# Kernel optimization log

Hardware: AMD Instinct MI355X
Metric: run time of the kernel (lower is better)

## Reference

```python
import jax, jax.numpy as jnp
import numpy as np

B, NCOL, NCOND = 1024, 64, 64
NRODT, D, NEST, NFOREST, NHID, NCLASS = 1024, 4, 128, 100, 128, 10
EPS = 1e-5


def setup_inputs() -> dict:
    key = jax.random.key(0)
    ks = jax.random.split(key, 16)
    rng = np.random.default_rng(0)
    s = 0.1
    inp = {
        'x': jax.random.normal(ks[0], (B, NCOL), jnp.float32),
        # phi_1 numerical grouped conv: groups=NCOL, in_per_g=1, out_per_g=NCOND
        'w1': jax.random.normal(ks[1], (NCOL, 1, NCOND), jnp.float32) * s,
        'b1': jax.random.normal(ks[2], (NCOL * NCOND,), jnp.float32) * s,
        # rODTConstruction fixed permutation of the 4096 conditions
        'perm': jnp.asarray(rng.permutation(NCOND * NCOL), jnp.int32),
        'gn1_g': jnp.ones((NCOND * NCOL,), jnp.float32),
        'gn1_b': jnp.zeros((NCOND * NCOL,), jnp.float32),
        # phi_2 grouped convs: groups=NRODT, block D->D then D->1
        'w2a': jax.random.normal(ks[3], (NRODT, D, D), jnp.float32) * s,
        'b2a': jax.random.normal(ks[4], (NRODT * D,), jnp.float32) * s,
        'gn2_g': jnp.ones((NCOND * NCOL,), jnp.float32),
        'gn2_b': jnp.zeros((NCOND * NCOL,), jnp.float32),
        'w2b': jax.random.normal(ks[5], (NRODT, D, 1), jnp.float32) * s,
        'b2b': jax.random.normal(ks[6], (NRODT,), jnp.float32) * s,
        'E': jax.random.normal(ks[7], (NRODT, NHID), jnp.float32) * s,
        # eval-mode sample_without_replacement buffer: per-forest subset of rODTs
        'swr': jnp.asarray(np.argsort(rng.random((NFOREST, NRODT)), axis=-1)[:, :NEST], jnp.int32),
        'ln1_g': jnp.ones((NHID,), jnp.float32),
        'ln1_b': jnp.zeros((NHID,), jnp.float32),
        'lin1_w': jax.random.normal(ks[8], (NHID, NHID), jnp.float32) * s,
        'lin1_b': jax.random.normal(ks[9], (NHID,), jnp.float32) * s,
        'ln2_g': jnp.ones((NHID,), jnp.float32),
        'ln2_b': jnp.zeros((NHID,), jnp.float32),
        'lin2_w': jax.random.normal(ks[10], (NHID, NCLASS), jnp.float32) * s,
        'lin2_b': jax.random.normal(ks[11], (NCLASS,), jnp.float32) * s,
    }
    return inp


def _group_norm(v, g, gamma, beta):
    # v: (B, C), normalize within each of g channel groups (L=1 in the torch module)
    b, c = v.shape
    vg = v.reshape(b, g, c // g)
    mu = vg.mean(-1, keepdims=True)
    var = vg.var(-1, keepdims=True)
    vn = ((vg - mu) / jnp.sqrt(var + EPS)).reshape(b, c)
    return vn * gamma + beta


def _layer_norm(v, gamma, beta):
    mu = v.mean(-1, keepdims=True)
    var = v.var(-1, keepdims=True)
    return (v - mu) / jnp.sqrt(var + EPS) * gamma + beta


def reference(x, w1, b1, perm, gn1_g, gn1_b, w2a, b2a, gn2_g, gn2_b, w2b, b2b,
              E, swr, ln1_g, ln1_b, lin1_w, lin1_b, ln2_g, ln2_b, lin2_w, lin2_b):
    b = x.shape[0]
    # ConditionGeneration (numerical only): block-diag GEMV with in_per_group=1
    M = jax.nn.sigmoid(x[:, :, None] * w1[None, :, 0, :] + b1.reshape(NCOL, NCOND))  # (B, NCOL, NCOND)
    M = M.transpose(0, 2, 1)  # (B, NCOND, NCOL)
    # rODTConstruction: flatten + fixed permutation
    O = M.reshape(b, NCOND * NCOL)[:, perm]  # (B, 4096)
    # phi_2: GroupNorm -> grouped conv (D->D) -> ReLU -> GroupNorm -> grouped conv (D->1)
    h = _group_norm(O, NRODT, gn1_g, gn1_b).reshape(b, NRODT, D)
    h = jnp.einsum('bgi,gio->bgo', h, w2a) + b2a.reshape(NRODT, D)
    h = jax.nn.relu(h).reshape(b, NRODT * D)
    h = _group_norm(h, NRODT, gn2_g, gn2_b).reshape(b, NRODT, D)
    w = jnp.einsum('bgi,gio->bgo', h, w2b)[..., 0] + b2b  # (B, NRODT), n_head=1
    # forest construction: gather rODT subsets, softmax over estimators, weighted embed sum
    ws = jax.nn.softmax(w[:, swr], axis=-1)  # (B, NFOREST, NEST)
    Es = E[swr]  # (NFOREST, NEST, NHID)
    F = jnp.einsum('bfe,feh->bfh', ws, Es)  # (B, NFOREST, NHID)
    # phi_3 bagging MLP (eval mode: dropout = identity)
    z = _layer_norm(F, ln1_g, ln1_b)
    z = jax.nn.relu(z @ lin1_w + lin1_b)
    z = _layer_norm(z, ln2_g, ln2_b)
    y_hats = z @ lin2_w + lin2_b  # (B, NFOREST, NCLASS)
    return y_hats.mean(1)  # (B, NCLASS)
```

## Files before the change

kernel.cpp:

```cpp
#include <hip/hip_runtime.h>


#define B_      1024
#define NCOL_   64
#define NCOND_  64
#define NRODT_  1024
#define NEST_   128
#define NFOREST_ 100
#define NHID_   128
#define NCLASS_ 10
#define EPS_    1e-5f

typedef __bf16 bf16_t;
typedef bf16_t bf16x8 __attribute__((ext_vector_type(8)));
typedef float  f32x4  __attribute__((ext_vector_type(4)));

#define MFMA16(a,b,c) __builtin_amdgcn_mfma_f32_16x16x32_bf16(a,b,c,0,0,0)

#define EG_FRAGS   (NFOREST_*4*8*64)
#define W1_FRAGS   (4*8*64)
#define L2_FRAGS   (4*64)

__global__ __launch_bounds__(256) void k_prep(
    const float* __restrict__ E,     const int*   __restrict__ swr,
    const float* __restrict__ lin1w, const float* __restrict__ lin2w,
    const float* __restrict__ x,
    bf16_t* __restrict__ Eh,  bf16_t* __restrict__ El,
    bf16_t* __restrict__ Wh,  bf16_t* __restrict__ Wl,
    bf16_t* __restrict__ L2h, bf16_t* __restrict__ L2l,
    float*  __restrict__ x_t, float* __restrict__ accz)
{
    int blk = blockIdx.x, tid = threadIdx.x;
    if (blk < 800) {
        int t = blk * 256 + tid;
        int lane = t & 63, nn = (t >> 6) & 7, kk = (t >> 9) & 3, f = t >> 11;
        int q = lane >> 4, n = nn * 16 + (lane & 15);
        bf16x8 hi, lo;
#pragma unroll
        for (int j = 0; j < 8; ++j) {
            int e = kk * 32 + q * 8 + j;
            int r = swr[f * NEST_ + e];
            float v = E[r * NHID_ + n];
            bf16_t h = (bf16_t)v;
            hi[j] = h; lo[j] = (bf16_t)(v - (float)h);
        }
        *(bf16x8*)(Eh + (size_t)t * 8) = hi;
        *(bf16x8*)(El + (size_t)t * 8) = lo;
    } else if (blk < 808) {
        int t = (blk - 800) * 256 + tid;
        int lane = t & 63, nn = (t >> 6) & 7, kk = t >> 9;
        int q = lane >> 4, n = nn * 16 + (lane & 15);
        bf16x8 hi, lo;
#pragma unroll
        for (int j = 0; j < 8; ++j) {
            int k = kk * 32 + q * 8 + j;
            float v = lin1w[k * NHID_ + n];
            bf16_t h = (bf16_t)v;
            hi[j] = h; lo[j] = (bf16_t)(v - (float)h);
        }
        *(bf16x8*)(Wh + t * 8) = hi;
        *(bf16x8*)(Wl + t * 8) = lo;
    } else if (blk == 808) {
        int t = tid;
        int lane = t & 63, kk = t >> 6;
        int q = lane >> 4, n = lane & 15;
        bf16x8 hi, lo;
#pragma unroll
        for (int j = 0; j < 8; ++j) {
            int k = kk * 32 + q * 8 + j;
            float v = (n < NCLASS_) ? lin2w[k * NCLASS_ + n] : 0.f;
            bf16_t h = (bf16_t)v;
            hi[j] = h; lo[j] = (bf16_t)(v - (float)h);
        }
        *(bf16x8*)(L2h + t * 8) = hi;
        *(bf16x8*)(L2l + t * 8) = lo;
    } else if (blk < 1065) {
        int t = (blk - 809) * 256 + tid;
        x_t[t] = x[(t & 1023) * NCOL_ + (t >> 10)];
    } else {
        int t = (blk - 1065) * 256 + tid;
        if (t < B_ * NCLASS_) accz[t] = 0.f;
    }
}

__global__ __launch_bounds__(256) void k_rodt(
    const float* __restrict__ x_t,  const float* __restrict__ w1,
    const float* __restrict__ b1,   const int*  __restrict__ perm,
    const float* __restrict__ gn1g, const float* __restrict__ gn1b,
    const float* __restrict__ w2a,  const float* __restrict__ b2a,
    const float* __restrict__ gn2g, const float* __restrict__ gn2b,
    const float* __restrict__ w2b,  const float* __restrict__ b2b,
    float* __restrict__ w_t)
{
    int g  = blockIdx.x;
    int bq = threadIdx.x * 4;

    int4 p4 = ((const int4*)perm)[g];
    int col[4]  = { p4.x & 63, p4.y & 63, p4.z & 63, p4.w & 63 };
    int cond[4] = { p4.x >> 6, p4.y >> 6, p4.z >> 6, p4.w >> 6 };
    float w1v[4], b1v[4];
#pragma unroll
    for (int j = 0; j < 4; ++j) {
        w1v[j] = w1[col[j] * NCOND_ + cond[j]];
        b1v[j] = b1[col[j] * NCOND_ + cond[j]];
    }
    float4 g1  = ((const float4*)gn1g)[g];
    float4 o1  = ((const float4*)gn1b)[g];
    float4 ba  = ((const float4*)b2a)[g];
    float4 g2  = ((const float4*)gn2g)[g];
    float4 o2  = ((const float4*)gn2b)[g];
    float4 wb4 = ((const float4*)w2b)[g];
    float  bb  = b2b[g];
    float4 wa[4];
    const float4* w2a4 = (const float4*)w2a;
#pragma unroll
    for (int i = 0; i < 4; ++i) wa[i] = w2a4[g * 4 + i];

    float xv[4][4];
#pragma unroll
    for (int j = 0; j < 4; ++j) {
        float4 t = *(const float4*)&x_t[col[j] * B_ + bq];
        xv[j][0] = t.x; xv[j][1] = t.y; xv[j][2] = t.z; xv[j][3] = t.w;
    }

    float outv[4];
#pragma unroll
    for (int bi = 0; bi < 4; ++bi) {
        float v[4];
#pragma unroll
        for (int j = 0; j < 4; ++j) {
            float t = xv[j][bi] * w1v[j] + b1v[j];
            v[j] = 1.0f / (1.0f + __expf(-t));
        }
        float mu = (v[0] + v[1] + v[2] + v[3]) * 0.25f;
        float var = 0.f;
#pragma unroll
        for (int j = 0; j < 4; ++j) { float d = v[j] - mu; var += d * d; }
        var *= 0.25f;
        float rs = rsqrtf(var + EPS_);
        float h[4];
        h[0] = (v[0] - mu) * rs * g1.x + o1.x;
        h[1] = (v[1] - mu) * rs * g1.y + o1.y;
        h[2] = (v[2] - mu) * rs * g1.z + o1.z;
        h[3] = (v[3] - mu) * rs * g1.w + o1.w;

        float4 a = ba;
#pragma unroll
        for (int i = 0; i < 4; ++i) {
            a.x += h[i] * wa[i].x; a.y += h[i] * wa[i].y;
            a.z += h[i] * wa[i].z; a.w += h[i] * wa[i].w;
        }
        float t2[4];
        t2[0] = fmaxf(a.x, 0.f); t2[1] = fmaxf(a.y, 0.f);
        t2[2] = fmaxf(a.z, 0.f); t2[3] = fmaxf(a.w, 0.f);

        float mu2 = (t2[0] + t2[1] + t2[2] + t2[3]) * 0.25f;
        float var2 = 0.f;
#pragma unroll
        for (int j = 0; j < 4; ++j) { float d = t2[j] - mu2; var2 += d * d; }
        var2 *= 0.25f;
        float rs2 = rsqrtf(var2 + EPS_);

        float wvv = bb;
        wvv += ((t2[0] - mu2) * rs2 * g2.x + o2.x) * wb4.x;
        wvv += ((t2[1] - mu2) * rs2 * g2.y + o2.y) * wb4.y;
        wvv += ((t2[2] - mu2) * rs2 * g2.z + o2.z) * wb4.z;
        wvv += ((t2[3] - mu2) * rs2 * g2.w + o2.w) * wb4.w;
        outv[bi] = wvv;
    }
    *(float4*)&w_t[(size_t)g * B_ + bq] = make_float4(outv[0], outv[1], outv[2], outv[3]);
}

__global__ __launch_bounds__(256, 4) void k_forest(
    const float*  __restrict__ w_t, const int* __restrict__ swr,
    const bf16_t* __restrict__ Eh,  const bf16_t* __restrict__ El,
    const bf16_t* __restrict__ Wh,  const bf16_t* __restrict__ Wl,
    const bf16_t* __restrict__ L2h, const bf16_t* __restrict__ L2l,
    const float* __restrict__ ln1g, const float* __restrict__ ln1b,
    const float* __restrict__ lin1b,
    const float* __restrict__ ln2g, const float* __restrict__ ln2b,
    float* __restrict__ acc)
{
    __shared__ float zsh[4][16 * 132];

    int tid  = threadIdx.x;
    int wid  = tid >> 6;
    int lane = tid & 63;
    int q    = lane >> 4;
    int mc   = lane & 15;

    int n    = blockIdx.x;
    int swiz = (n & 7) * 200 + (n >> 3);
    int f    = swiz >> 4;
    int bt   = swiz & 15;
    int b0   = bt * 64 + wid * 16;

    const int* swrf = swr + f * NEST_;
    float* zw = zsh[wid];

    float ex[4][8];
    float mx = -1e30f;
#pragma unroll
    for (int kk = 0; kk < 4; ++kk) {
        int4 r0 = *(const int4*)(swrf + kk * 32 + q * 8);
        int4 r1 = *(const int4*)(swrf + kk * 32 + q * 8 + 4);
        int rr[8] = { r0.x, r0.y, r0.z, r0.w, r1.x, r1.y, r1.z, r1.w };
#pragma unroll
        for (int j = 0; j < 8; ++j) {
            float v = w_t[rr[j] * B_ + b0 + mc];
            ex[kk][j] = v;
            mx = fmaxf(mx, v);
        }
    }
    mx = fmaxf(mx, __shfl_xor(mx, 16));
    mx = fmaxf(mx, __shfl_xor(mx, 32));
    float s = 0.f;
#pragma unroll
    for (int kk = 0; kk < 4; ++kk)
#pragma unroll
        for (int j = 0; j < 8; ++j) { ex[kk][j] = __expf(ex[kk][j] - mx); s += ex[kk][j]; }
    s += __shfl_xor(s, 16);
    s += __shfl_xor(s, 32);
    float inv = 1.f / s;

    bf16x8 afr[4];
#pragma unroll
    for (int kk = 0; kk < 4; ++kk)
#pragma unroll
        for (int j = 0; j < 8; ++j) afr[kk][j] = (bf16_t)(ex[kk][j] * inv);

    f32x4 accF[8];
#pragma unroll
    for (int nn = 0; nn < 8; ++nn) accF[nn] = (f32x4){0.f, 0.f, 0.f, 0.f};
    const bf16x8* EHf = (const bf16x8*)Eh;
    const bf16x8* ELf = (const bf16x8*)El;
#pragma unroll
    for (int kk = 0; kk < 4; ++kk) {
        size_t bi = (size_t)(f * 4 + kk) * 8;
#pragma unroll
        for (int nn = 0; nn < 8; ++nn) {
            bf16x8 bh = EHf[(bi + nn) * 64 + lane];
            bf16x8 bl = ELf[(bi + nn) * 64 + lane];
            accF[nn] = MFMA16(afr[kk], bh, accF[nn]);
            accF[nn] = MFMA16(afr[kk], bl, accF[nn]);
        }
    }

    float mu[4], rs[4];
#pragma unroll
    for (int reg = 0; reg < 4; ++reg) {
        float ps = 0.f, pq = 0.f;
#pragma unroll
        for (int nn = 0; nn < 8; ++nn) { float v = accF[nn][reg]; ps += v; pq += v * v; }
#pragma unroll
        for (int o = 1; o <= 8; o <<= 1) { ps += __shfl_xor(ps, o); pq += __shfl_xor(pq, o); }
        float m_ = ps * (1.f / NHID_);
        mu[reg] = m_;
        rs[reg] = rsqrtf(pq * (1.f / NHID_) - m_ * m_ + EPS_);
    }
    {
#pragma unroll
        for (int nn = 0; nn < 8; ++nn) {
            int c = nn * 16 + mc;
            float gv = ln1g[c], bv = ln1b[c];
#pragma unroll
            for (int reg = 0; reg < 4; ++reg)
                zw[(q * 4 + reg) * 132 + c] = (accF[nn][reg] - mu[reg]) * rs[reg] * gv + bv;
        }
    }

    bf16x8 a2[4];
#pragma unroll
    for (int kk = 0; kk < 4; ++kk) {
        int dwb = kk * 32 + q * 8;
        f32x4 u0 = *(const f32x4*)&zw[mc * 132 + dwb];
        f32x4 u1 = *(const f32x4*)&zw[mc * 132 + dwb + 4];
#pragma unroll
        for (int j = 0; j < 4; ++j) { a2[kk][j] = (bf16_t)u0[j]; a2[kk][4 + j] = (bf16_t)u1[j]; }
    }
    f32x4 accA[8];
#pragma unroll
    for (int nn = 0; nn < 8; ++nn) accA[nn] = (f32x4){0.f, 0.f, 0.f, 0.f};
    const bf16x8* WHf = (const bf16x8*)Wh;
    const bf16x8* WLf = (const bf16x8*)Wl;
#pragma unroll
    for (int kk = 0; kk < 4; ++kk) {
#pragma unroll
        for (int nn = 0; nn < 8; ++nn) {
            bf16x8 bh = WHf[(kk * 8 + nn) * 64 + lane];
            bf16x8 bl = WLf[(kk * 8 + nn) * 64 + lane];
            accA[nn] = MFMA16(a2[kk], bh, accA[nn]);
            accA[nn] = MFMA16(a2[kk], bl, accA[nn]);
        }
    }

#pragma unroll
    for (int nn = 0; nn < 8; ++nn) {
        float bv = lin1b[nn * 16 + mc];
#pragma unroll
        for (int reg = 0; reg < 4; ++reg)
            accA[nn][reg] = fmaxf(accA[nn][reg] + bv, 0.f);
    }
    float mu2[4], rs2[4];
#pragma unroll
    for (int reg = 0; reg < 4; ++reg) {
        float ps = 0.f, pq = 0.f;
#pragma unroll
        for (int nn = 0; nn < 8; ++nn) { float v = accA[nn][reg]; ps += v; pq += v * v; }
#pragma unroll
        for (int o = 1; o <= 8; o <<= 1) { ps += __shfl_xor(ps, o); pq += __shfl_xor(pq, o); }
        float m_ = ps * (1.f / NHID_);
        mu2[reg] = m_;
        rs2[reg] = rsqrtf(pq * (1.f / NHID_) - m_ * m_ + EPS_);
    }
    {
#pragma unroll
        for (int nn = 0; nn < 8; ++nn) {
            int c = nn * 16 + mc;
            float gv = ln2g[c], bv = ln2b[c];
#pragma unroll
            for (int reg = 0; reg < 4; ++reg)
                zw[(q * 4 + reg) * 132 + c] = (accA[nn][reg] - mu2[reg]) * rs2[reg] * gv + bv;
        }
    }

    f32x4 accO = {0.f, 0.f, 0.f, 0.f};
    const bf16x8* LHf = (const bf16x8*)L2h;
    const bf16x8* LLf = (const bf16x8*)L2l;
#pragma unroll
    for (int kk = 0; kk < 4; ++kk) {
        int dwb = kk * 32 + q * 8;
        f32x4 u0 = *(const f32x4*)&zw[mc * 132 + dwb];
        f32x4 u1 = *(const f32x4*)&zw[mc * 132 + dwb + 4];
        bf16x8 a3;
#pragma unroll
        for (int j = 0; j < 4; ++j) { a3[j] = (bf16_t)u0[j]; a3[4 + j] = (bf16_t)u1[j]; }
        accO = MFMA16(a3, LHf[kk * 64 + lane], accO);
        accO = MFMA16(a3, LLf[kk * 64 + lane], accO);
    }
    if (mc < NCLASS_) {
#pragma unroll
        for (int reg = 0; reg < 4; ++reg)
            atomicAdd(&acc[(b0 + q * 4 + reg) * NCLASS_ + mc], accO[reg]);
    }
}

__global__ __launch_bounds__(256) void k_final(
    const float* __restrict__ acc, const float* __restrict__ lin2b,
    float* __restrict__ out)
{
    int i = blockIdx.x * 256 + threadIdx.x;
    if (i < B_ * NCLASS_) {
        int c = i % NCLASS_;
        out[i] = acc[i] * (1.f / NFOREST_) + lin2b[c];
    }
}

extern "C" void kernel_launch(void* const* d_in, const int* in_sizes, int n_in,
                              void* d_out, int out_size, void* d_ws, size_t ws_size,
                              hipStream_t stream)
{
    const float* x     = (const float*)d_in[0];
    const float* w1    = (const float*)d_in[1];
    const float* b1    = (const float*)d_in[2];
    const int*   perm  = (const int*)  d_in[3];
    const float* gn1g  = (const float*)d_in[4];
    const float* gn1b  = (const float*)d_in[5];
    const float* w2a   = (const float*)d_in[6];
    const float* b2a   = (const float*)d_in[7];
    const float* gn2g  = (const float*)d_in[8];
    const float* gn2b  = (const float*)d_in[9];
    const float* w2b   = (const float*)d_in[10];
    const float* b2b   = (const float*)d_in[11];
    const float* E     = (const float*)d_in[12];
    const int*   swr   = (const int*)  d_in[13];
    const float* ln1g  = (const float*)d_in[14];
    const float* ln1b  = (const float*)d_in[15];
    const float* lin1w = (const float*)d_in[16];
    const float* lin1b = (const float*)d_in[17];
    const float* ln2g  = (const float*)d_in[18];
    const float* ln2b  = (const float*)d_in[19];
    const float* lin2w = (const float*)d_in[20];
    const float* lin2b = (const float*)d_in[21];

    char* base = (char*)d_ws;
    float*  w_t  = (float*)base;
    float*  accp = (float*)(base + 4u * 1024 * 1024);
    float*  x_t  = (float*)(base + 4u * 1024 * 1024 + 64 * 1024);
    bf16_t* Eh   = (bf16_t*)(base + 4u * 1024 * 1024 + 64 * 1024 + 256 * 1024);
    bf16_t* El   = Eh  + (size_t)EG_FRAGS * 8;
    bf16_t* Wh   = El  + (size_t)EG_FRAGS * 8;
    bf16_t* Wl   = Wh  + (size_t)W1_FRAGS * 8;
    bf16_t* L2h  = Wl  + (size_t)W1_FRAGS * 8;
    bf16_t* L2l  = L2h + (size_t)L2_FRAGS * 8;

    k_prep<<<1105, 256, 0, stream>>>(E, swr, lin1w, lin2w, x,
                                     Eh, El, Wh, Wl, L2h, L2l, x_t, accp);

    k_rodt<<<NRODT_, 256, 0, stream>>>(
        x_t, w1, b1, perm, gn1g, gn1b, w2a, b2a, gn2g, gn2b, w2b, b2b, w_t);

    k_forest<<<NFOREST_ * 16, 256, 0, stream>>>(
        w_t, swr, Eh, El, Wh, Wl, L2h, L2l,
        ln1g, ln1b, lin1b, ln2g, ln2b, accp);

    k_final<<<(B_ * NCLASS_ + 255) / 256, 256, 0, stream>>>(
        accp, lin2b, (float*)d_out);
}
```

Baseline: 150.3 us.

## Merge weight prep into rODT kernel, drop final kernel, store bf16 activations in LDS

Moves the E/lin1/lin2 bf16 hi/lo splitting into the same launch as the rODT computation, so the independent work overlaps and one launch goes away. The output is initialised with the bias up front and the forest kernel atomically adds pre-scaled partial results directly into it, removing the accumulator buffer and the final kernel. The LDS staging between MLP layers now holds bf16 instead of float, which halves shared memory, and the occupancy hint rises from 4 to 8 blocks per CU. The bf16 conversion now happens before the LDS store rather than after, so numerics stay the same, while scaling before the atomic slightly changes rounding order.

After: 179.7 us. 1.2x slower.

```diff
diff --git a/kernel.cpp b/kernel.cpp
--- a/kernel.cpp
+++ b/kernel.cpp
@@ -20,70 +20,28 @@
 #define EG_FRAGS   (NFOREST_*4*8*64)
 #define W1_FRAGS   (4*8*64)
 #define L2_FRAGS   (4*64)
-
-__global__ __launch_bounds__(256) void k_prep(
+#define ZPAD_      136
+
+__global__ __launch_bounds__(256) void k_pre(
+    const float* __restrict__ x, const float* __restrict__ lin2b,
+    float* __restrict__ x_t, float* __restrict__ out)
+{
+    int blk = blockIdx.x, tid = threadIdx.x;
+    if (blk < 256) {
+        int t = blk * 256 + tid;
+        x_t[t] = x[(t & 1023) * NCOL_ + (t >> 10)];
+    } else {
+        int t = (blk - 256) * 256 + tid;
+        if (t < B_ * NCLASS_) out[t] = lin2b[t % NCLASS_];
+    }
+}
+
+__global__ __launch_bounds__(256) void k_main(
     const float* __restrict__ E,     const int*   __restrict__ swr,
     const float* __restrict__ lin1w, const float* __restrict__ lin2w,
-    const float* __restrict__ x,
     bf16_t* __restrict__ Eh,  bf16_t* __restrict__ El,
     bf16_t* __restrict__ Wh,  bf16_t* __restrict__ Wl,
     bf16_t* __restrict__ L2h, bf16_t* __restrict__ L2l,
-    float*  __restrict__ x_t, float* __restrict__ accz)
-{
-    int blk = blockIdx.x, tid = threadIdx.x;
-    if (blk < 800) {
-        int t = blk * 256 + tid;
-        int lane = t & 63, nn = (t >> 6) & 7, kk = (t >> 9) & 3, f = t >> 11;
-        int q = lane >> 4, n = nn * 16 + (lane & 15);
-        bf16x8 hi, lo;
-#pragma unroll
-        for (int j = 0; j < 8; ++j) {
-            int e = kk * 32 + q * 8 + j;
-            int r = swr[f * NEST_ + e];
-            float v = E[r * NHID_ + n];
-            bf16_t h = (bf16_t)v;
-            hi[j] = h; lo[j] = (bf16_t)(v - (float)h);
-        }
-        *(bf16x8*)(Eh + (size_t)t * 8) = hi;
-        *(bf16x8*)(El + (size_t)t * 8) = lo;
-    } else if (blk < 808) {
-        int t = (blk - 800) * 256 + tid;
-        int lane = t & 63, nn = (t >> 6) & 7, kk = t >> 9;
-        int q = lane >> 4, n = nn * 16 + (lane & 15);
-        bf16x8 hi, lo;
-#pragma unroll
-        for (int j = 0; j < 8; ++j) {
-            int k = kk * 32 + q * 8 + j;
-            float v = lin1w[k * NHID_ + n];
-            bf16_t h = (bf16_t)v;
-            hi[j] = h; lo[j] = (bf16_t)(v - (float)h);
-        }
-        *(bf16x8*)(Wh + t * 8) = hi;
-        *(bf16x8*)(Wl + t * 8) = lo;
-    } else if (blk == 808) {
-        int t = tid;
-        int lane = t & 63, kk = t >> 6;
-        int q = lane >> 4, n = lane & 15;
-        bf16x8 hi, lo;
-#pragma unroll
-        for (int j = 0; j < 8; ++j) {
-            int k = kk * 32 + q * 8 + j;
-            float v = (n < NCLASS_) ? lin2w[k * NCLASS_ + n] : 0.f;
-            bf16_t h = (bf16_t)v;
-            hi[j] = h; lo[j] = (bf16_t)(v - (float)h);
-        }
-        *(bf16x8*)(L2h + t * 8) = hi;
-        *(bf16x8*)(L2l + t * 8) = lo;
-    } else if (blk < 1065) {
-        int t = (blk - 809) * 256 + tid;
-        x_t[t] = x[(t & 1023) * NCOL_ + (t >> 10)];
-    } else {
-        int t = (blk - 1065) * 256 + tid;
-        if (t < B_ * NCLASS_) accz[t] = 0.f;
-    }
-}
-
-__global__ __launch_bounds__(256) void k_rodt(
     const float* __restrict__ x_t,  const float* __restrict__ w1,
     const float* __restrict__ b1,   const int*  __restrict__ perm,
     const float* __restrict__ gn1g, const float* __restrict__ gn1b,
@@ -92,8 +50,59 @@
     const float* __restrict__ w2b,  const float* __restrict__ b2b,
     float* __restrict__ w_t)
 {
-    int g  = blockIdx.x;
-    int bq = threadIdx.x * 4;
+    int blk = blockIdx.x, tid = threadIdx.x;
+    if (blk < 800) {
+        int t = blk * 256 + tid;
+        int lane = t & 63, nn = (t >> 6) & 7, kk = (t >> 9) & 3, f = t >> 11;
+        int q = lane >> 4, n = nn * 16 + (lane & 15);
+        bf16x8 hi, lo;
+#pragma unroll
+        for (int j = 0; j < 8; ++j) {
+            int e = kk * 32 + q * 8 + j;
+            int r = swr[f * NEST_ + e];
+            float v = E[r * NHID_ + n];
+            bf16_t h = (bf16_t)v;
+            hi[j] = h; lo[j] = (bf16_t)(v - (float)h);
+        }
+        *(bf16x8*)(Eh + (size_t)t * 8) = hi;
+        *(bf16x8*)(El + (size_t)t * 8) = lo;
+        return;
+    }
+    if (blk < 808) {
+        int t = (blk - 800) * 256 + tid;
+        int lane = t & 63, nn = (t >> 6) & 7, kk = t >> 9;
+        int q = lane >> 4, n = nn * 16 + (lane & 15);
+        bf16x8 hi, lo;
+#pragma unroll
+        for (int j = 0; j < 8; ++j) {
+            int k = kk * 32 + q * 8 + j;
+            float v = lin1w[k * NHID_ + n];
+            bf16_t h = (bf16_t)v;
+            hi[j] = h; lo[j] = (bf16_t)(v - (float)h);
+        }
+        *(bf16x8*)(Wh + t * 8) = hi;
+        *(bf16x8*)(Wl + t * 8) = lo;
+        return;
+    }
+    if (blk == 808) {
+        int t = tid;
+        int lane = t & 63, kk = t >> 6;
+        int q = lane >> 4, n = lane & 15;
+        bf16x8 hi, lo;
+#pragma unroll
+        for (int j = 0; j < 8; ++j) {
+            int k = kk * 32 + q * 8 + j;
+            float v = (n < NCLASS_) ? lin2w[k * NCLASS_ + n] : 0.f;
+            bf16_t h = (bf16_t)v;
+            hi[j] = h; lo[j] = (bf16_t)(v - (float)h);
+        }
+        *(bf16x8*)(L2h + t * 8) = hi;
+        *(bf16x8*)(L2l + t * 8) = lo;
+        return;
+    }
+
+    int g  = blk - 809;
+    int bq = tid * 4;
 
     int4 p4 = ((const int4*)perm)[g];
     int col[4]  = { p4.x & 63, p4.y & 63, p4.z & 63, p4.w & 63 };
@@ -171,7 +180,7 @@
     *(float4*)&w_t[(size_t)g * B_ + bq] = make_float4(outv[0], outv[1], outv[2], outv[3]);
 }
 
-__global__ __launch_bounds__(256, 4) void k_forest(
+__global__ __launch_bounds__(256, 8) void k_forest(
     const float*  __restrict__ w_t, const int* __restrict__ swr,
     const bf16_t* __restrict__ Eh,  const bf16_t* __restrict__ El,
     const bf16_t* __restrict__ Wh,  const bf16_t* __restrict__ Wl,
@@ -179,9 +188,9 @@
     const float* __restrict__ ln1g, const float* __restrict__ ln1b,
     const float* __restrict__ lin1b,
     const float* __restrict__ ln2g, const float* __restrict__ ln2b,
-    float* __restrict__ acc)
+    float* __restrict__ out)
 {
-    __shared__ float zsh[4][16 * 132];
+    __shared__ bf16_t zsh[4][16 * ZPAD_];
 
     int tid  = threadIdx.x;
     int wid  = tid >> 6;
@@ -196,7 +205,7 @@
     int b0   = bt * 64 + wid * 16;
 
     const int* swrf = swr + f * NEST_;
-    float* zw = zsh[wid];
+    bf16_t* zw = zsh[wid];
 
     float ex[4][8];
     float mx = -1e30f;
@@ -258,26 +267,20 @@
         mu[reg] = m_;
         rs[reg] = rsqrtf(pq * (1.f / NHID_) - m_ * m_ + EPS_);
     }
-    {
-#pragma unroll
-        for (int nn = 0; nn < 8; ++nn) {
-            int c = nn * 16 + mc;
-            float gv = ln1g[c], bv = ln1b[c];
-#pragma unroll
-            for (int reg = 0; reg < 4; ++reg)
-                zw[(q * 4 + reg) * 132 + c] = (accF[nn][reg] - mu[reg]) * rs[reg] * gv + bv;
-        }
+#pragma unroll
+    for (int nn = 0; nn < 8; ++nn) {
+        int c = nn * 16 + mc;
+        float gv = ln1g[c], bv = ln1b[c];
+#pragma unroll
+        for (int reg = 0; reg < 4; ++reg)
+            zw[(q * 4 + reg) * ZPAD_ + c] =
+                (bf16_t)((accF[nn][reg] - mu[reg]) * rs[reg] * gv + bv);
     }
 
     bf16x8 a2[4];
 #pragma unroll
-    for (int kk = 0; kk < 4; ++kk) {
-        int dwb = kk * 32 + q * 8;
-        f32x4 u0 = *(const f32x4*)&zw[mc * 132 + dwb];
-        f32x4 u1 = *(const f32x4*)&zw[mc * 132 + dwb + 4];
-#pragma unroll
-        for (int j = 0; j < 4; ++j) { a2[kk][j] = (bf16_t)u0[j]; a2[kk][4 + j] = (bf16_t)u1[j]; }
-    }
+    for (int kk = 0; kk < 4; ++kk)
+        a2[kk] = *(const bf16x8*)&zw[mc * ZPAD_ + kk * 32 + q * 8];
     f32x4 accA[8];
 #pragma unroll
     for (int nn = 0; nn < 8; ++nn) accA[nn] = (f32x4){0.f, 0.f, 0.f, 0.f};
@@ -313,15 +316,14 @@
         mu2[reg] = m_;
         rs2[reg] = rsqrtf(pq * (1.f / NHID_) - m_ * m_ + EPS_);
     }
-    {
-#pragma unroll
-        for (int nn = 0; nn < 8; ++nn) {
-            int c = nn * 16 + mc;
-            float gv = ln2g[c], bv = ln2b[c];
-#pragma unroll
-            for (int reg = 0; reg < 4; ++reg)
-                zw[(q * 4 + reg) * 132 + c] = (accA[nn][reg] - mu2[reg]) * rs2[reg] * gv + bv;
-        }
+#pragma unroll
+    for (int nn = 0; nn < 8; ++nn) {
+        int c = nn * 16 + mc;
+        float gv = ln2g[c], bv = ln2b[c];
+#pragma unroll
+        for (int reg = 0; reg < 4; ++reg)
+            zw[(q * 4 + reg) * ZPAD_ + c] =
+                (bf16_t)((accA[nn][reg] - mu2[reg]) * rs2[reg] * gv + bv);
     }
 
     f32x4 accO = {0.f, 0.f, 0.f, 0.f};
@@ -329,30 +331,15 @@
     const bf16x8* LLf = (const bf16x8*)L2l;
 #pragma unroll
     for (int kk = 0; kk < 4; ++kk) {
-        int dwb = kk * 32 + q * 8;
-        f32x4 u0 = *(const f32x4*)&zw[mc * 132 + dwb];
-        f32x4 u1 = *(const f32x4*)&zw[mc * 132 + dwb + 4];
-        bf16x8 a3;
-#pragma unroll
-        for (int j = 0; j < 4; ++j) { a3[j] = (bf16_t)u0[j]; a3[4 + j] = (bf16_t)u1[j]; }
+        bf16x8 a3 = *(const bf16x8*)&zw[mc * ZPAD_ + kk * 32 + q * 8];
         accO = MFMA16(a3, LHf[kk * 64 + lane], accO);
         accO = MFMA16(a3, LLf[kk * 64 + lane], accO);
     }
     if (mc < NCLASS_) {
 #pragma unroll
         for (int reg = 0; reg < 4; ++reg)
-            atomicAdd(&acc[(b0 + q * 4 + reg) * NCLASS_ + mc], accO[reg]);
-    }
-}
-
-__global__ __launch_bounds__(256) void k_final(
-    const float* __restrict__ acc, const float* __restrict__ lin2b,
-    float* __restrict__ out)
-{
-    int i = blockIdx.x * 256 + threadIdx.x;
-    if (i < B_ * NCLASS_) {
-        int c = i % NCLASS_;
-        out[i] = acc[i] * (1.f / NFOREST_) + lin2b[c];
+            atomicAdd(&out[(b0 + q * 4 + reg) * NCLASS_ + mc],
+                      accO[reg] * (1.f / NFOREST_));
     }
 }
 
@@ -385,25 +372,24 @@
 
     char* base = (char*)d_ws;
     float*  w_t  = (float*)base;
-    float*  accp = (float*)(base + 4u * 1024 * 1024);
-    float*  x_t  = (float*)(base + 4u * 1024 * 1024 + 64 * 1024);
-    bf16_t* Eh   = (bf16_t*)(base + 4u * 1024 * 1024 + 64 * 1024 + 256 * 1024);
+    float*  x_t  = (float*)(base + 4u * 1024 * 1024);
+    bf16_t* Eh   = (bf16_t*)(base + 4u * 1024 * 1024 + 256 * 1024);
     bf16_t* El   = Eh  + (size_t)EG_FRAGS * 8;
     bf16_t* Wh   = El  + (size_t)EG_FRAGS * 8;
     bf16_t* Wl   = Wh  + (size_t)W1_FRAGS * 8;
     bf16_t* L2h  = Wl  + (size_t)W1_FRAGS * 8;
     bf16_t* L2l  = L2h + (size_t)L2_FRAGS * 8;
 
-    k_prep<<<1105, 256, 0, stream>>>(E, swr, lin1w, lin2w, x,
-                                     Eh, El, Wh, Wl, L2h, L2l, x_t, accp);
-
-    k_rodt<<<NRODT_, 256, 0, stream>>>(
-        x_t, w1, b1, perm, gn1g, gn1b, w2a, b2a, gn2g, gn2b, w2b, b2b, w_t);
+    float* outp = (float*)d_out;
+
+    k_pre<<<296, 256, 0, stream>>>(x, lin2b, x_t, outp);
+
+    k_main<<<1833, 256, 0, stream>>>(E, swr, lin1w, lin2w,
+                                     Eh, El, Wh, Wl, L2h, L2l,
+                                     x_t, w1, b1, perm, gn1g, gn1b,
+                                     w2a, b2a, gn2g, gn2b, w2b, b2b, w_t);
 
     k_forest<<<NFOREST_ * 16, 256, 0, stream>>>(
         w_t, swr, Eh, El, Wh, Wl, L2h, L2l,
-        ln1g, ln1b, lin1b, ln2g, ln2b, accp);
-
-    k_final<<<(B_ * NCLASS_ + 255) / 256, 256, 0, stream>>>(
-        accp, lin2b, (float*)d_out);
+        ln1g, ln1b, lin1b, ln2g, ln2b, outp);
 }
```
